# Performance work log

Measured on AMD Instinct MI355X. Metric: run time of the kernel, lower is better.

## Reference

```python
import jax, jax.numpy as jnp
import numpy as np

NEG = float(-2**32 + 1)  # mask fill value used by the original module
H = 8  # number of heads (matches init kwarg h)


def setup_inputs() -> dict:
    key = jax.random.key(0)
    B, S, D, Q, V = 4, 2048, 512, 64, 64
    ks = jax.random.split(key, 10)
    sc = 1.0 / np.sqrt(D)
    x = jax.random.normal(ks[0], (B, S, D), jnp.float32)
    padding_mask = jax.random.randint(ks[1], (B, S), 0, 2, jnp.int32)
    Wq = jax.random.normal(ks[2], (H * Q, D), jnp.float32) * sc
    bq = jnp.zeros((H * Q,), jnp.float32)
    Wk = jax.random.normal(ks[3], (H * Q, D), jnp.float32) * sc
    bk = jnp.zeros((H * Q,), jnp.float32)
    Wv = jax.random.normal(ks[4], (H * V, D), jnp.float32) * sc
    bv = jnp.zeros((H * V,), jnp.float32)
    Wo = jax.random.normal(ks[5], (D, H * V), jnp.float32) * (1.0 / np.sqrt(H * V))
    bo = jnp.zeros((D,), jnp.float32)
    return {"x": x, "padding_mask": padding_mask, "Wq": Wq, "bq": bq,
            "Wk": Wk, "bk": bk, "Wv": Wv, "bv": bv, "Wo": Wo, "bo": bo}


def reference(x, padding_mask, Wq, bq, Wk, bk, Wv, bv, Wo, bo):
    # stage is hardcoded to 'train' (mask=True in init), so the causal branch runs.
    B, S, D = x.shape
    q_dim = Wq.shape[0] // H
    v_dim = Wv.shape[0] // H

    def split_heads(t, d):
        # torch: cat(chunk(h, dim=-1), dim=0) -> head-major [H*B, S, d]
        return t.reshape(B, S, H, d).transpose(2, 0, 1, 3).reshape(H * B, S, d)

    Qh = split_heads(x @ Wq.T + bq, q_dim)   # [H*B, S, q]
    Kh = split_heads(x @ Wk.T + bk, q_dim)
    Vh = split_heads(x @ Wv.T + bv, v_dim)

    score = jnp.einsum('nsd,ntd->nst', Qh, Kh) / jnp.sqrt(jnp.float32(q_dim))  # [H*B,S,S]
    pre_score = score  # module returns the UNMASKED scores (saved before masking)

    # causal mask (mask=True, stage=='train')
    causal = jnp.tril(jnp.ones((S, S), jnp.float32))
    score = jnp.where(causal > 0, score, NEG)

    # padding mask: built batch-major [B*H,S,S] while score is head-major [H*B,...]
    # -- faithful reproduction of the original ordering quirk.
    pm = jnp.broadcast_to(padding_mask[:, None, None, :], (B, H, S, S)).reshape(B * H, S, S)
    score = jnp.where(pm == 0, NEG, score)

    attn = jax.nn.softmax(score, axis=-1)
    out = jnp.einsum('nst,ntd->nsd', attn, Vh)  # [H*B, S, v]

    # torch: cat(chunk(h, dim=0), dim=-1) -> [B, S, H*v]
    heads = out.reshape(H, B, S, v_dim).transpose(1, 2, 0, 3).reshape(B, S, H * v_dim)
    self_attention = heads @ Wo.T + bo
    return self_attention, pre_score
```

## Files before the change

### kernel.cpp

```cpp
#include <hip/hip_runtime.h>
#include <hip/hip_fp16.h>
#include <math.h>

typedef _Float16 f16;
typedef _Float16 f16x8 __attribute__((ext_vector_type(8)));
typedef _Float16 f16x4 __attribute__((ext_vector_type(4)));
typedef float    f32x4 __attribute__((ext_vector_type(4)));

#define MFMA16(a,b,c) __builtin_amdgcn_mfma_f32_16x16x32_f16(a, b, c, 0, 0, 0)

#define MASKNEG (-6.0e9f)
#define DEADTHR (-1.0e9f)
#define LOG2E   1.44269504088896f

__global__ __launch_bounds__(256) void qkv_gemm(
    const float* __restrict__ x,
    const float* __restrict__ Wq, const float* __restrict__ bq,
    const float* __restrict__ Wk, const float* __restrict__ bk,
    const float* __restrict__ Wv, const float* __restrict__ bv,
    f16* __restrict__ Qws, f16* __restrict__ Kws, f16* __restrict__ Vt)
{
    __shared__ f16 Al[128 * 48];
    __shared__ f16 Wl[64 * 48];

    const int tid = threadIdx.x;
    const int bx  = blockIdx.x;
    const int m0  = blockIdx.y * 128;
    const int widx = bx >> 3;
    const int n0   = (bx & 7) * 64;

    const float* W    = (widx == 0) ? Wq : (widx == 1) ? Wk : Wv;
    const float* bias = (widx == 0) ? bq : (widx == 1) ? bk : bv;
    const float scl  = (widx == 0) ? 0.125f : 1.0f;

    const int wid = tid >> 6, lane = tid & 63;
    const int g = lane >> 4, c = lane & 15;
    const int wm = (wid >> 1) * 64, wn = (wid & 1) * 32;
    const int sr = tid >> 3, sc = tid & 7;

    f32x4 acc[4][2] = {};

    for (int kk = 0; kk < 512; kk += 32) {
        __syncthreads();
        #pragma unroll
        for (int rr = 0; rr < 4; ++rr) {
            int row = sr + rr * 32;
            float4 v = *(const float4*)&x[(size_t)(m0 + row) * 512 + kk + sc * 4];
            f16x4 h4 = {(f16)v.x, (f16)v.y, (f16)v.z, (f16)v.w};
            *(f16x4*)&Al[row * 48 + sc * 4] = h4;
        }
        #pragma unroll
        for (int rr = 0; rr < 2; ++rr) {
            int row = sr + rr * 32;
            float4 v = *(const float4*)&W[(size_t)(n0 + row) * 512 + kk + sc * 4];
            f16x4 h4 = {(f16)v.x, (f16)v.y, (f16)v.z, (f16)v.w};
            *(f16x4*)&Wl[row * 48 + sc * 4] = h4;
        }
        __syncthreads();

        f16x8 b0 = *(const f16x8*)&Wl[(wn +  0 + c) * 48 + g * 8];
        f16x8 b1 = *(const f16x8*)&Wl[(wn + 16 + c) * 48 + g * 8];
        #pragma unroll
        for (int mf = 0; mf < 4; ++mf) {
            f16x8 a = *(const f16x8*)&Al[(wm + mf * 16 + c) * 48 + g * 8];
            acc[mf][0] = MFMA16(a, b0, acc[mf][0]);
            acc[mf][1] = MFMA16(a, b1, acc[mf][1]);
        }
    }

    #pragma unroll
    for (int nf = 0; nf < 2; ++nf) {
        int cc = n0 + wn + nf * 16 + c;
        float bval = bias[cc];
        #pragma unroll
        for (int mf = 0; mf < 4; ++mf) {
            if (widx < 2) {
                f16* outp = (widx == 0) ? Qws : Kws;
                #pragma unroll
                for (int r = 0; r < 4; ++r) {
                    int mrow = m0 + wm + mf * 16 + g * 4 + r;
                    outp[(size_t)mrow * 512 + cc] = (f16)((acc[mf][nf][r] + bval) * scl);
                }
            } else {
                int h  = n0 >> 6;
                int d  = wn + nf * 16 + c;
                int t0 = m0 + wm + mf * 16 + g * 4;
                int b  = t0 >> 11;
                int ts = t0 & 2047;
                int nn = h * 4 + b;
                f16x4 pk = {(f16)(acc[mf][nf][0] + bval), (f16)(acc[mf][nf][1] + bval),
                            (f16)(acc[mf][nf][2] + bval), (f16)(acc[mf][nf][3] + bval)};
                *(f16x4*)&Vt[((size_t)(nn * 64 + d)) * 2048 + ts] = pk;
            }
        }
    }
}

__global__ __launch_bounds__(256) void vsum_kernel(
    const f16* __restrict__ Vt, float* __restrict__ Vsum)
{
    const int row  = blockIdx.x * 4 + (threadIdx.x >> 6);
    const int lane = threadIdx.x & 63;
    const f16* p = Vt + (size_t)row * 2048;
    float s = 0.f;
    #pragma unroll
    for (int i = 0; i < 4; ++i) {
        f16x8 v = *(const f16x8*)&p[i * 512 + lane * 8];
        #pragma unroll
        for (int j = 0; j < 8; ++j) s += (float)v[j];
    }
    #pragma unroll
    for (int off = 1; off < 64; off <<= 1) s += __shfl_xor(s, off, 64);
    if (lane == 0) Vsum[row] = s;
}

__global__ __launch_bounds__(256) void attn_kernel(
    const f16* __restrict__ Qws, const f16* __restrict__ Kws,
    const f16* __restrict__ Vt,  const int* __restrict__ pmask,
    const float* __restrict__ Vsum,
    float* __restrict__ pre_score, f16* __restrict__ attn_out)
{
    __shared__ f16 Kl[64 * 72];
    __shared__ f16 Vl[64 * 72];
    __shared__ f16 Pl[4][32 * 72];
    __shared__ float Bias[2048];

    const int tid = threadIdx.x;
    const int wid = tid >> 6, lane = tid & 63;
    const int g = lane >> 4, c = lane & 15;
    const int qt = blockIdx.x;
    const int n  = blockIdx.y;
    const int h = n >> 2, b = n & 3;
    const int pmrow = n >> 3;
    const int qlo = qt * 64 + wid * 16;
    const int qhi = (31 - qt) * 64 + wid * 16;
    const int qrel = wid * 16 + c;

    {
        const int i0 = tid * 8;
        const int4* p4 = (const int4*)(pmask + pmrow * 2048 + i0);
        int4 m0 = p4[0], m1 = p4[1];
        Bias[i0 + 0] = m0.x ? 0.f : MASKNEG;
        Bias[i0 + 1] = m0.y ? 0.f : MASKNEG;
        Bias[i0 + 2] = m0.z ? 0.f : MASKNEG;
        Bias[i0 + 3] = m0.w ? 0.f : MASKNEG;
        Bias[i0 + 4] = m1.x ? 0.f : MASKNEG;
        Bias[i0 + 5] = m1.y ? 0.f : MASKNEG;
        Bias[i0 + 6] = m1.z ? 0.f : MASKNEG;
        Bias[i0 + 7] = m1.w ? 0.f : MASKNEG;
    }

    f16x8 qf[2][2];
    #pragma unroll
    for (int ks = 0; ks < 2; ++ks) {
        qf[0][ks] = *(const f16x8*)
            &Qws[(size_t)(b * 2048 + qlo + c) * 512 + h * 64 + ks * 32 + g * 8];
        qf[1][ks] = *(const f16x8*)
            &Qws[(size_t)(b * 2048 + qhi + c) * 512 + h * 64 + ks * 32 + g * 8];
    }

    f32x4 o[2][4] = {};
    float mrow[2] = {-INFINITY, -INFINITY};
    float lrow[2] = {0.f, 0.f};

    const int sr = tid >> 3, sc = tid & 7;
    const f16* Kbase = Kws + (size_t)(b * 2048) * 512 + h * 64;
    const f16* Vbase = Vt + (size_t)(n * 64) * 2048;
    float* prow0 = pre_score + ((size_t)n * 2048 + qlo + c) * 2048;
    float* prow1 = pre_score + ((size_t)n * 2048 + qhi + c) * 2048;

    const int stageEnd = 32 - qt;

    uint4 ka0, ka1, va0, va1;
    auto glbload = [&](int kt) {
        ka0 = *(const uint4*)&Kbase[(size_t)(kt * 64 + sr) * 512 + sc * 8];
        ka1 = *(const uint4*)&Kbase[(size_t)(kt * 64 + sr + 32) * 512 + sc * 8];
        va0 = *(const uint4*)&Vbase[(size_t)sr * 2048 + kt * 64 + sc * 8];
        va1 = *(const uint4*)&Vbase[(size_t)(sr + 32) * 2048 + kt * 64 + sc * 8];
    };

    glbload(0);
    for (int kt = 0; kt < stageEnd; ++kt) {
        asm volatile("s_waitcnt lgkmcnt(0)" ::: "memory");
        __builtin_amdgcn_s_barrier();
        *(uint4*)&Kl[sr * 72 + sc * 8]        = ka0;
        *(uint4*)&Kl[(sr + 32) * 72 + sc * 8] = ka1;
        *(uint4*)&Vl[sr * 72 + sc * 8]        = va0;
        *(uint4*)&Vl[(sr + 32) * 72 + sc * 8] = va1;
        asm volatile("s_waitcnt lgkmcnt(0)" ::: "memory");
        __builtin_amdgcn_s_barrier();
        if (kt + 1 < stageEnd) glbload(kt + 1);

        f32x4 s2[2][4] = {};
        #pragma unroll
        for (int kc = 0; kc < 4; ++kc)
            #pragma unroll
            for (int ks = 0; ks < 2; ++ks) {
                f16x8 kf = *(const f16x8*)&Kl[(kc * 16 + c) * 72 + ks * 32 + g * 8];
                s2[0][kc] = MFMA16(kf, qf[0][ks], s2[0][kc]);
                s2[1][kc] = MFMA16(kf, qf[1][ks], s2[1][kc]);
            }

        #pragma unroll
        for (int kc = 0; kc < 4; ++kc) {
            *(f32x4*)&prow0[kt * 64 + kc * 16 + g * 4] = s2[0][kc];
            *(f32x4*)&prow1[kt * 64 + kc * 16 + g * 4] = s2[1][kc];
        }

        f32x4 bi[4];
        #pragma unroll
        for (int kc = 0; kc < 4; ++kc)
            bi[kc] = *(const f32x4*)&Bias[kt * 64 + kc * 16 + g * 4];

        const bool L0 = (kt <= qt);
        const bool bnd0 = (kt == qt), bnd1 = (kt == 31 - qt);

        #pragma unroll
        for (int mi = 0; mi < 2; ++mi) {
            if (mi == 0 && !L0) continue;
            const bool bnd = mi ? bnd1 : bnd0;
            float sl[4][4];
            #pragma unroll
            for (int kc = 0; kc < 4; ++kc)
                #pragma unroll
                for (int r = 0; r < 4; ++r) {
                    float sv = s2[mi][kc][r] + bi[kc][r];
                    int klocal = kc * 16 + g * 4 + r;
                    sl[kc][r] = (bnd && klocal > qrel) ? MASKNEG : sv;
                }
            float rm = sl[0][0];
            #pragma unroll
            for (int kc = 0; kc < 4; ++kc)
                #pragma unroll
                for (int r = 0; r < 4; ++r) rm = fmaxf(rm, sl[kc][r]);
            rm = fmaxf(rm, __shfl_xor(rm, 16, 64));
            rm = fmaxf(rm, __shfl_xor(rm, 32, 64));
            float mn = fmaxf(mrow[mi], rm);
            float alpha = exp2f((mrow[mi] - mn) * LOG2E);
            mrow[mi] = mn;
            float ml2 = mn * LOG2E;
            float rs = 0.f;
            #pragma unroll
            for (int kc = 0; kc < 4; ++kc) {
                f16x4 pk;
                #pragma unroll
                for (int r = 0; r < 4; ++r) {
                    float p = exp2f(fmaf(sl[kc][r], LOG2E, -ml2));
                    rs += p;
                    pk[r] = (f16)p;
                }
                *(f16x4*)&Pl[wid][(mi * 16 + c) * 72 + kc * 16 + g * 4] = pk;
            }
            rs += __shfl_xor(rs, 16, 64);
            rs += __shfl_xor(rs, 32, 64);
            lrow[mi] = lrow[mi] * alpha + rs;
            #pragma unroll
            for (int r = 0; r < 4; ++r) {
                float af = __shfl(alpha, g * 4 + r, 64);
                #pragma unroll
                for (int dn = 0; dn < 4; ++dn) o[mi][dn][r] *= af;
            }
        }
        asm volatile("s_waitcnt lgkmcnt(0)" ::: "memory");

        #pragma unroll
        for (int ks = 0; ks < 2; ++ks) {
            f16x8 pa0, pa1;
            if (L0) pa0 = *(const f16x8*)&Pl[wid][( 0 + c) * 72 + ks * 32 + g * 8];
            pa1 = *(const f16x8*)&Pl[wid][(16 + c) * 72 + ks * 32 + g * 8];
            #pragma unroll
            for (int dn = 0; dn < 4; ++dn) {
                f16x8 vb = *(const f16x8*)&Vl[(dn * 16 + c) * 72 + ks * 32 + g * 8];
                if (L0) o[0][dn] = MFMA16(pa0, vb, o[0][dn]);
                o[1][dn] = MFMA16(pa1, vb, o[1][dn]);
            }
        }
    }

    for (int kt = stageEnd; kt < 32; ++kt) {
        f32x4 s2[2][4] = {};
        #pragma unroll
        for (int kc = 0; kc < 4; ++kc)
            #pragma unroll
            for (int ks = 0; ks < 2; ++ks) {
                f16x8 kf = *(const f16x8*)
                    &Kbase[(size_t)(kt * 64 + kc * 16 + c) * 512 + ks * 32 + g * 8];
                s2[0][kc] = MFMA16(kf, qf[0][ks], s2[0][kc]);
                s2[1][kc] = MFMA16(kf, qf[1][ks], s2[1][kc]);
            }
        #pragma unroll
        for (int kc = 0; kc < 4; ++kc) {
            *(f32x4*)&prow0[kt * 64 + kc * 16 + g * 4] = s2[0][kc];
            *(f32x4*)&prow1[kt * 64 + kc * 16 + g * 4] = s2[1][kc];
        }
    }

    #pragma unroll
    for (int mi = 0; mi < 2; ++mi) {
        int qb = mi ? qhi : qlo;
        #pragma unroll
        for (int r = 0; r < 4; ++r) {
            float lo = __shfl(lrow[mi], g * 4 + r, 64);
            float mo = __shfl(mrow[mi], g * 4 + r, 64);
            int srow = qb + g * 4 + r;
            bool dead = (mo < DEADTHR);
            float inv_l = dead ? 0.f : 1.0f / lo;
            #pragma unroll
            for (int dn = 0; dn < 4; ++dn) {
                float val = dead ? Vsum[n * 64 + dn * 16 + c] * (1.0f / 2048.0f)
                                 : o[mi][dn][r] * inv_l;
                attn_out[(size_t)(b * 2048 + srow) * 512 + h * 64 + dn * 16 + c] = (f16)val;
            }
        }
    }
}

__global__ __launch_bounds__(256) void out_gemm(
    const f16* __restrict__ Aattn, const float* __restrict__ Wo,
    const float* __restrict__ bo, float* __restrict__ outp)
{
    __shared__ f16 Al[128 * 48];
    __shared__ f16 Wl[64 * 48];

    const int tid = threadIdx.x;
    const int n0 = blockIdx.x * 64;
    const int m0 = blockIdx.y * 128;
    const int wid = tid >> 6, lane = tid & 63;
    const int g = lane >> 4, c = lane & 15;
    const int wm = (wid >> 1) * 64, wn = (wid & 1) * 32;

    const int sr4 = tid >> 2, sc4 = tid & 3;
    const int sr8 = tid >> 3, sc8 = tid & 7;

    f32x4 acc[4][2] = {};

    for (int kk = 0; kk < 512; kk += 32) {
        __syncthreads();
        #pragma unroll
        for (int rr = 0; rr < 2; ++rr) {
            int row = sr4 + rr * 64;
            *(uint4*)&Al[row * 48 + sc4 * 8] =
                *(const uint4*)&Aattn[(size_t)(m0 + row) * 512 + kk + sc4 * 8];
        }
        #pragma unroll
        for (int rr = 0; rr < 2; ++rr) {
            int row = sr8 + rr * 32;
            float4 v = *(const float4*)&Wo[(size_t)(n0 + row) * 512 + kk + sc8 * 4];
            f16x4 h4 = {(f16)v.x, (f16)v.y, (f16)v.z, (f16)v.w};
            *(f16x4*)&Wl[row * 48 + sc8 * 4] = h4;
        }
        __syncthreads();

        f16x8 b0 = *(const f16x8*)&Wl[(wn +  0 + c) * 48 + g * 8];
        f16x8 b1 = *(const f16x8*)&Wl[(wn + 16 + c) * 48 + g * 8];
        #pragma unroll
        for (int mf = 0; mf < 4; ++mf) {
            f16x8 a = *(const f16x8*)&Al[(wm + mf * 16 + c) * 48 + g * 8];
            acc[mf][0] = MFMA16(a, b0, acc[mf][0]);
            acc[mf][1] = MFMA16(a, b1, acc[mf][1]);
        }
    }

    #pragma unroll
    for (int nf = 0; nf < 2; ++nf) {
        int cc = n0 + wn + nf * 16 + c;
        float bval = bo[cc];
        #pragma unroll
        for (int mf = 0; mf < 4; ++mf)
            #pragma unroll
            for (int r = 0; r < 4; ++r)
                outp[(size_t)(m0 + wm + mf * 16 + g * 4 + r) * 512 + cc] =
                    acc[mf][nf][r] + bval;
    }
}

extern "C" void kernel_launch(void* const* d_in, const int* in_sizes, int n_in,
                              void* d_out, int out_size, void* d_ws, size_t ws_size,
                              hipStream_t stream)
{
    (void)in_sizes; (void)n_in; (void)out_size; (void)ws_size;

    const float* x  = (const float*)d_in[0];
    const int*   pm = (const int*)  d_in[1];
    const float* Wq = (const float*)d_in[2];
    const float* bq = (const float*)d_in[3];
    const float* Wk = (const float*)d_in[4];
    const float* bk = (const float*)d_in[5];
    const float* Wv = (const float*)d_in[6];
    const float* bv = (const float*)d_in[7];
    const float* Wo = (const float*)d_in[8];
    const float* bo = (const float*)d_in[9];

    float* out = (float*)d_out;
    float* pre = out + (size_t)4 * 2048 * 512;

    f16*   Qws  = (f16*)d_ws;
    f16*   Kws  = Qws + (size_t)8192 * 512;
    f16*   Vt   = Kws + (size_t)8192 * 512;
    f16*   Aat  = Vt  + (size_t)2048 * 2048;
    float* Vsum = (float*)(Aat + (size_t)8192 * 512);

    qkv_gemm   <<<dim3(24, 64), 256, 0, stream>>>(x, Wq, bq, Wk, bk, Wv, bv, Qws, Kws, Vt);
    vsum_kernel<<<dim3(512),    256, 0, stream>>>(Vt, Vsum);
    attn_kernel<<<dim3(16, 32), 256, 0, stream>>>(Qws, Kws, Vt, pm, Vsum, pre, Aat);
    out_gemm   <<<dim3(8, 64),  256, 0, stream>>>(Aat, Wo, bo, out);
}
```

Measured before the change: 286.0 us.

## Split attention KV loop across two blocks and merge partials in combine kernel

The attention kernel gains a z-dimension of 2, so each block handles every other key tile (split-K / flash-decoding style), doubling the grid from 512 to 1024 blocks. Each block writes unnormalized fp16 partial outputs plus per-row max and sum into a workspace, and a new combine kernel rescales and merges them, applying the dead-row Vsum fallback. Softmax+PV is refactored into a per-row-chunk lambda with a smaller P buffer, and launch bounds request 3 blocks per SM. This aims to fill the GPU better at the cost of an extra kernel launch, partial-buffer traffic, fp16 rounding of unnormalized partials, and per-block setup (bias, Q load) being repeated.

```diff
diff --git a/kernel.cpp b/kernel.cpp
--- a/kernel.cpp
+++ b/kernel.cpp
@@ -114,15 +114,14 @@
     if (lane == 0) Vsum[row] = s;
 }
 
-__global__ __launch_bounds__(256) void attn_kernel(
+__global__ __launch_bounds__(256, 3) void attn_kernel(
     const f16* __restrict__ Qws, const f16* __restrict__ Kws,
     const f16* __restrict__ Vt,  const int* __restrict__ pmask,
-    const float* __restrict__ Vsum,
-    float* __restrict__ pre_score, f16* __restrict__ attn_out)
+    float* __restrict__ pre_score, f16* __restrict__ part)
 {
     __shared__ f16 Kl[64 * 72];
     __shared__ f16 Vl[64 * 72];
-    __shared__ f16 Pl[4][32 * 72];
+    __shared__ f16 Pl[4][16 * 72];
     __shared__ float Bias[2048];
 
     const int tid = threadIdx.x;
@@ -130,6 +129,7 @@
     const int g = lane >> 4, c = lane & 15;
     const int qt = blockIdx.x;
     const int n  = blockIdx.y;
+    const int p  = blockIdx.z;
     const int h = n >> 2, b = n & 3;
     const int pmrow = n >> 3;
     const int qlo = qt * 64 + wid * 16;
@@ -179,8 +179,63 @@
         va1 = *(const uint4*)&Vbase[(size_t)(sr + 32) * 2048 + kt * 64 + sc * 8];
     };
 
-    glbload(0);
-    for (int kt = 0; kt < stageEnd; ++kt) {
+    auto chunk_sm_pv = [&](int mi, bool bnd, const f32x4* s2c, const f32x4* bi)
+        __attribute__((always_inline)) {
+        float sl[4][4];
+        #pragma unroll
+        for (int kc = 0; kc < 4; ++kc)
+            #pragma unroll
+            for (int r = 0; r < 4; ++r) {
+                float sv = s2c[kc][r] + bi[kc][r];
+                int klocal = kc * 16 + g * 4 + r;
+                sl[kc][r] = (bnd && klocal > qrel) ? MASKNEG : sv;
+            }
+        float rm = sl[0][0];
+        #pragma unroll
+        for (int kc = 0; kc < 4; ++kc)
+            #pragma unroll
+            for (int r = 0; r < 4; ++r) rm = fmaxf(rm, sl[kc][r]);
+        rm = fmaxf(rm, __shfl_xor(rm, 16, 64));
+        rm = fmaxf(rm, __shfl_xor(rm, 32, 64));
+        float mn = fmaxf(mrow[mi], rm);
+        float alpha = exp2f((mrow[mi] - mn) * LOG2E);
+        mrow[mi] = mn;
+        float ml2 = mn * LOG2E;
+        float rs = 0.f;
+        #pragma unroll
+        for (int kc = 0; kc < 4; ++kc) {
+            f16x4 pk;
+            #pragma unroll
+            for (int r = 0; r < 4; ++r) {
+                float pe = exp2f(fmaf(sl[kc][r], LOG2E, -ml2));
+                rs += pe;
+                pk[r] = (f16)pe;
+            }
+            *(f16x4*)&Pl[wid][c * 72 + kc * 16 + g * 4] = pk;
+        }
+        rs += __shfl_xor(rs, 16, 64);
+        rs += __shfl_xor(rs, 32, 64);
+        lrow[mi] = lrow[mi] * alpha + rs;
+        #pragma unroll
+        for (int r = 0; r < 4; ++r) {
+            float af = __shfl(alpha, g * 4 + r, 64);
+            #pragma unroll
+            for (int dn = 0; dn < 4; ++dn) o[mi][dn][r] *= af;
+        }
+        asm volatile("s_waitcnt lgkmcnt(0)" ::: "memory");
+        #pragma unroll
+        for (int ks = 0; ks < 2; ++ks) {
+            f16x8 pa = *(const f16x8*)&Pl[wid][c * 72 + ks * 32 + g * 8];
+            #pragma unroll
+            for (int dn = 0; dn < 4; ++dn) {
+                f16x8 vb = *(const f16x8*)&Vl[(dn * 16 + c) * 72 + ks * 32 + g * 8];
+                o[mi][dn] = MFMA16(pa, vb, o[mi][dn]);
+            }
+        }
+    };
+
+    glbload(p);
+    for (int kt = p; kt < stageEnd; kt += 2) {
         asm volatile("s_waitcnt lgkmcnt(0)" ::: "memory");
         __builtin_amdgcn_s_barrier();
         *(uint4*)&Kl[sr * 72 + sc * 8]        = ka0;
@@ -189,7 +244,7 @@
         *(uint4*)&Vl[(sr + 32) * 72 + sc * 8] = va1;
         asm volatile("s_waitcnt lgkmcnt(0)" ::: "memory");
         __builtin_amdgcn_s_barrier();
-        if (kt + 1 < stageEnd) glbload(kt + 1);
+        if (kt + 2 < stageEnd) glbload(kt + 2);
 
         f32x4 s2[2][4] = {};
         #pragma unroll
@@ -213,71 +268,12 @@
             bi[kc] = *(const f32x4*)&Bias[kt * 64 + kc * 16 + g * 4];
 
         const bool L0 = (kt <= qt);
-        const bool bnd0 = (kt == qt), bnd1 = (kt == 31 - qt);
-
-        #pragma unroll
-        for (int mi = 0; mi < 2; ++mi) {
-            if (mi == 0 && !L0) continue;
-            const bool bnd = mi ? bnd1 : bnd0;
-            float sl[4][4];
-            #pragma unroll
-            for (int kc = 0; kc < 4; ++kc)
-                #pragma unroll
-                for (int r = 0; r < 4; ++r) {
-                    float sv = s2[mi][kc][r] + bi[kc][r];
-                    int klocal = kc * 16 + g * 4 + r;
-                    sl[kc][r] = (bnd && klocal > qrel) ? MASKNEG : sv;
-                }
-            float rm = sl[0][0];
-            #pragma unroll
-            for (int kc = 0; kc < 4; ++kc)
-                #pragma unroll
-                for (int r = 0; r < 4; ++r) rm = fmaxf(rm, sl[kc][r]);
-            rm = fmaxf(rm, __shfl_xor(rm, 16, 64));
-            rm = fmaxf(rm, __shfl_xor(rm, 32, 64));
-            float mn = fmaxf(mrow[mi], rm);
-            float alpha = exp2f((mrow[mi] - mn) * LOG2E);
-            mrow[mi] = mn;
-            float ml2 = mn * LOG2E;
-            float rs = 0.f;
-            #pragma unroll
-            for (int kc = 0; kc < 4; ++kc) {
-                f16x4 pk;
-                #pragma unroll
-                for (int r = 0; r < 4; ++r) {
-                    float p = exp2f(fmaf(sl[kc][r], LOG2E, -ml2));
-                    rs += p;
-                    pk[r] = (f16)p;
-                }
-                *(f16x4*)&Pl[wid][(mi * 16 + c) * 72 + kc * 16 + g * 4] = pk;
-            }
-            rs += __shfl_xor(rs, 16, 64);
-            rs += __shfl_xor(rs, 32, 64);
-            lrow[mi] = lrow[mi] * alpha + rs;
-            #pragma unroll
-            for (int r = 0; r < 4; ++r) {
-                float af = __shfl(alpha, g * 4 + r, 64);
-                #pragma unroll
-                for (int dn = 0; dn < 4; ++dn) o[mi][dn][r] *= af;
-            }
-        }
+        if (L0) chunk_sm_pv(0, kt == qt, s2[0], bi);
         asm volatile("s_waitcnt lgkmcnt(0)" ::: "memory");
-
-        #pragma unroll
-        for (int ks = 0; ks < 2; ++ks) {
-            f16x8 pa0, pa1;
-            if (L0) pa0 = *(const f16x8*)&Pl[wid][( 0 + c) * 72 + ks * 32 + g * 8];
-            pa1 = *(const f16x8*)&Pl[wid][(16 + c) * 72 + ks * 32 + g * 8];
-            #pragma unroll
-            for (int dn = 0; dn < 4; ++dn) {
-                f16x8 vb = *(const f16x8*)&Vl[(dn * 16 + c) * 72 + ks * 32 + g * 8];
-                if (L0) o[0][dn] = MFMA16(pa0, vb, o[0][dn]);
-                o[1][dn] = MFMA16(pa1, vb, o[1][dn]);
-            }
-        }
-    }
-
-    for (int kt = stageEnd; kt < 32; ++kt) {
+        chunk_sm_pv(1, kt == 31 - qt, s2[1], bi);
+    }
+
+    for (int kt = stageEnd + ((stageEnd ^ p) & 1); kt < 32; kt += 2) {
         f32x4 s2[2][4] = {};
         #pragma unroll
         for (int kc = 0; kc < 4; ++kc)
@@ -295,24 +291,64 @@
         }
     }
 
+    f16* pb = part + (size_t)p * 65536 * 72;
     #pragma unroll
     for (int mi = 0; mi < 2; ++mi) {
-        int qb = mi ? qhi : qlo;
-        #pragma unroll
-        for (int r = 0; r < 4; ++r) {
-            float lo = __shfl(lrow[mi], g * 4 + r, 64);
-            float mo = __shfl(mrow[mi], g * 4 + r, 64);
-            int srow = qb + g * 4 + r;
-            bool dead = (mo < DEADTHR);
-            float inv_l = dead ? 0.f : 1.0f / lo;
-            #pragma unroll
-            for (int dn = 0; dn < 4; ++dn) {
-                float val = dead ? Vsum[n * 64 + dn * 16 + c] * (1.0f / 2048.0f)
-                                 : o[mi][dn][r] * inv_l;
-                attn_out[(size_t)(b * 2048 + srow) * 512 + h * 64 + dn * 16 + c] = (f16)val;
-            }
-        }
-    }
+        size_t rowbase = (size_t)n * 2048 + (mi ? qhi : qlo);
+        #pragma unroll
+        for (int r = 0; r < 4; ++r)
+            #pragma unroll
+            for (int dn = 0; dn < 4; ++dn)
+                pb[(rowbase + g * 4 + r) * 72 + dn * 16 + c] = (f16)o[mi][dn][r];
+        if (g == 0) {
+            float* pf = (float*)&pb[(rowbase + c) * 72 + 64];
+            pf[0] = mrow[mi];
+            pf[1] = lrow[mi];
+        }
+    }
+}
+
+__global__ __launch_bounds__(256) void combine_kernel(
+    const f16* __restrict__ part, const float* __restrict__ Vsum,
+    f16* __restrict__ Aat)
+{
+    const int t  = threadIdx.x;
+    const int R  = blockIdx.x * 64 + (t >> 2);
+    const int dg = (t & 3) * 16;
+    const int n = R >> 11, q = R & 2047;
+    const int h = n >> 2, b = n & 3;
+    const f16* p0 = part + (size_t)R * 72;
+    const f16* p1 = part + ((size_t)65536 + R) * 72;
+    const float* ml0 = (const float*)(p0 + 64);
+    const float* ml1 = (const float*)(p1 + 64);
+    float m0 = ml0[0], l0 = ml0[1];
+    float m1 = ml1[0], l1 = ml1[1];
+    float m = fmaxf(m0, m1);
+    f16* outp = Aat + ((size_t)(b * 2048 + q)) * 512 + h * 64 + dg;
+    f16x8 r0, r1;
+    if (m < DEADTHR) {
+        const float* vs = Vsum + n * 64 + dg;
+        #pragma unroll
+        for (int i = 0; i < 8; ++i) {
+            r0[i] = (f16)(vs[i] * (1.0f / 2048.0f));
+            r1[i] = (f16)(vs[8 + i] * (1.0f / 2048.0f));
+        }
+    } else {
+        float w0 = (m0 < DEADTHR) ? 0.f : exp2f((m0 - m) * LOG2E);
+        float w1 = (m1 < DEADTHR) ? 0.f : exp2f((m1 - m) * LOG2E);
+        float invl = 1.0f / (l0 * w0 + l1 * w1);
+        f16x8 a0 = *(const f16x8*)&p0[dg];
+        f16x8 a1 = *(const f16x8*)&p0[dg + 8];
+        f16x8 c0 = *(const f16x8*)&p1[dg];
+        f16x8 c1 = *(const f16x8*)&p1[dg + 8];
+        #pragma unroll
+        for (int i = 0; i < 8; ++i) {
+            r0[i] = (f16)(((float)a0[i] * w0 + (float)c0[i] * w1) * invl);
+            r1[i] = (f16)(((float)a1[i] * w0 + (float)c1[i] * w1) * invl);
+        }
+    }
+    *(f16x8*)outp = r0;
+    *(f16x8*)(outp + 8) = r1;
 }
 
 __global__ __launch_bounds__(256) void out_gemm(
@@ -399,9 +435,11 @@
     f16*   Vt   = Kws + (size_t)8192 * 512;
     f16*   Aat  = Vt  + (size_t)2048 * 2048;
     float* Vsum = (float*)(Aat + (size_t)8192 * 512);
+    f16*   part = (f16*)(Vsum + 2048);
 
     qkv_gemm   <<<dim3(24, 64), 256, 0, stream>>>(x, Wq, bq, Wk, bk, Wv, bv, Qws, Kws, Vt);
     vsum_kernel<<<dim3(512),    256, 0, stream>>>(Vt, Vsum);
-    attn_kernel<<<dim3(16, 32), 256, 0, stream>>>(Qws, Kws, Vt, pm, Vsum, pre, Aat);
+    attn_kernel<<<dim3(16, 32, 2), 256, 0, stream>>>(Qws, Kws, Vt, pm, pre, part);
+    combine_kernel<<<dim3(1024), 256, 0, stream>>>(part, Vsum, Aat);
     out_gemm   <<<dim3(8, 64),  256, 0, stream>>>(Aat, Wo, bo, out);
 }
```

Result: slower. 300.7 us (+5.1%).

## Split pre_score writing into separate blocks interleaved with attention blocks

Applied to the files above, without the earlier changes.

Attention blocks no longer write the unmasked score matrix. Instead, 8 of every 9 blocks in a single fused grid recompute QK^T tiles and stream them to pre_score, while every 9th block runs flash attention. The aim is to separate the store-bound pre_score traffic from the MFMA/softmax work and spread it across many more blocks. The cost is that QK^T is computed twice.

```diff
diff --git a/kernel.cpp b/kernel.cpp
--- a/kernel.cpp
+++ b/kernel.cpp
@@ -114,7 +114,7 @@
     if (lane == 0) Vsum[row] = s;
 }
 
-__global__ __launch_bounds__(256) void attn_kernel(
+__global__ __launch_bounds__(256) void fat_kernel(
     const f16* __restrict__ Qws, const f16* __restrict__ Kws,
     const f16* __restrict__ Vt,  const int* __restrict__ pmask,
     const float* __restrict__ Vsum,
@@ -125,11 +125,49 @@
     __shared__ f16 Pl[4][32 * 72];
     __shared__ float Bias[2048];
 
+    const int bid = blockIdx.x;
     const int tid = threadIdx.x;
     const int wid = tid >> 6, lane = tid & 63;
     const int g = lane >> 4, c = lane & 15;
-    const int qt = blockIdx.x;
-    const int n  = blockIdx.y;
+
+    if (bid % 9 != 0) {
+        const int sid = bid - bid / 9 - 1;
+        const int n  = sid >> 7;
+        const int q0 = ((sid >> 3) & 15) * 128;
+        const int t0 = (sid & 7) * 256 + wid * 64;
+        const int h = n >> 2, b = n & 3;
+
+        const f16* Qbase = Qws + (size_t)(b * 2048) * 512 + h * 64;
+        const f16* Kbase = Kws + (size_t)(b * 2048) * 512 + h * 64;
+        float* prow = pre_score + ((size_t)n * 2048 + q0 + c) * 2048;
+
+        f16x8 qf[8][2];
+        #pragma unroll
+        for (int qi = 0; qi < 8; ++qi)
+            #pragma unroll
+            for (int ks = 0; ks < 2; ++ks)
+                qf[qi][ks] = *(const f16x8*)
+                    &Qbase[(size_t)(q0 + qi * 16 + c) * 512 + ks * 32 + g * 8];
+
+        #pragma unroll
+        for (int tf = 0; tf < 4; ++tf) {
+            const int t = t0 + tf * 16;
+            f16x8 kf0 = *(const f16x8*)&Kbase[(size_t)(t + c) * 512 + g * 8];
+            f16x8 kf1 = *(const f16x8*)&Kbase[(size_t)(t + c) * 512 + 32 + g * 8];
+            #pragma unroll
+            for (int qi = 0; qi < 8; ++qi) {
+                f32x4 acc = {};
+                acc = MFMA16(kf0, qf[qi][0], acc);
+                acc = MFMA16(kf1, qf[qi][1], acc);
+                *(f32x4*)&prow[(size_t)(qi * 16) * 2048 + t + g * 4] = acc;
+            }
+        }
+        return;
+    }
+
+    const int fid = bid / 9;
+    const int qt = fid & 15;
+    const int n  = fid >> 4;
     const int h = n >> 2, b = n & 3;
     const int pmrow = n >> 3;
     const int qlo = qt * 64 + wid * 16;
@@ -166,8 +204,6 @@
     const int sr = tid >> 3, sc = tid & 7;
     const f16* Kbase = Kws + (size_t)(b * 2048) * 512 + h * 64;
     const f16* Vbase = Vt + (size_t)(n * 64) * 2048;
-    float* prow0 = pre_score + ((size_t)n * 2048 + qlo + c) * 2048;
-    float* prow1 = pre_score + ((size_t)n * 2048 + qhi + c) * 2048;
 
     const int stageEnd = 32 - qt;
 
@@ -201,12 +237,6 @@
                 s2[1][kc] = MFMA16(kf, qf[1][ks], s2[1][kc]);
             }
 
-        #pragma unroll
-        for (int kc = 0; kc < 4; ++kc) {
-            *(f32x4*)&prow0[kt * 64 + kc * 16 + g * 4] = s2[0][kc];
-            *(f32x4*)&prow1[kt * 64 + kc * 16 + g * 4] = s2[1][kc];
-        }
-
         f32x4 bi[4];
         #pragma unroll
         for (int kc = 0; kc < 4; ++kc)
@@ -277,24 +307,6 @@
         }
     }
 
-    for (int kt = stageEnd; kt < 32; ++kt) {
-        f32x4 s2[2][4] = {};
-        #pragma unroll
-        for (int kc = 0; kc < 4; ++kc)
-            #pragma unroll
-            for (int ks = 0; ks < 2; ++ks) {
-                f16x8 kf = *(const f16x8*)
-                    &Kbase[(size_t)(kt * 64 + kc * 16 + c) * 512 + ks * 32 + g * 8];
-                s2[0][kc] = MFMA16(kf, qf[0][ks], s2[0][kc]);
-                s2[1][kc] = MFMA16(kf, qf[1][ks], s2[1][kc]);
-            }
-        #pragma unroll
-        for (int kc = 0; kc < 4; ++kc) {
-            *(f32x4*)&prow0[kt * 64 + kc * 16 + g * 4] = s2[0][kc];
-            *(f32x4*)&prow1[kt * 64 + kc * 16 + g * 4] = s2[1][kc];
-        }
-    }
-
     #pragma unroll
     for (int mi = 0; mi < 2; ++mi) {
         int qb = mi ? qhi : qlo;
@@ -402,6 +414,6 @@
 
     qkv_gemm   <<<dim3(24, 64), 256, 0, stream>>>(x, Wq, bq, Wk, bk, Wv, bv, Qws, Kws, Vt);
     vsum_kernel<<<dim3(512),    256, 0, stream>>>(Vt, Vsum);
-    attn_kernel<<<dim3(16, 32), 256, 0, stream>>>(Qws, Kws, Vt, pm, Vsum, pre, Aat);
+    fat_kernel <<<dim3(4608),   256, 0, stream>>>(Qws, Kws, Vt, pm, Vsum, pre, Aat);
     out_gemm   <<<dim3(8, 64),  256, 0, stream>>>(Aat, Wo, bo, out);
 }
```

Result: slower. 380.3 us (+33.0%).

## Split pre-score output into a dedicated streaming score kernel separate from flash attention

Applied to the files above, without the earlier changes.

The unmasked score matrix write is moved out of the fused attention kernel into a separate kernel that recomputes QK^T across all key tiles and streams the results with nontemporal stores. The flash kernel now only does the masked softmax and PV product, so it no longer carries the heavy global score stores or the non-causal tail loop. In exchange, QK^T for the causal half is computed twice, and Q/K are read again by a separate launch.

```diff
diff --git a/kernel.cpp b/kernel.cpp
--- a/kernel.cpp
+++ b/kernel.cpp
@@ -114,11 +114,10 @@
     if (lane == 0) Vsum[row] = s;
 }
 
-__global__ __launch_bounds__(256) void attn_kernel(
+__global__ __launch_bounds__(256) void flash_kernel(
     const f16* __restrict__ Qws, const f16* __restrict__ Kws,
     const f16* __restrict__ Vt,  const int* __restrict__ pmask,
-    const float* __restrict__ Vsum,
-    float* __restrict__ pre_score, f16* __restrict__ attn_out)
+    const float* __restrict__ Vsum, f16* __restrict__ attn_out)
 {
     __shared__ f16 Kl[64 * 72];
     __shared__ f16 Vl[64 * 72];
@@ -166,8 +165,6 @@
     const int sr = tid >> 3, sc = tid & 7;
     const f16* Kbase = Kws + (size_t)(b * 2048) * 512 + h * 64;
     const f16* Vbase = Vt + (size_t)(n * 64) * 2048;
-    float* prow0 = pre_score + ((size_t)n * 2048 + qlo + c) * 2048;
-    float* prow1 = pre_score + ((size_t)n * 2048 + qhi + c) * 2048;
 
     const int stageEnd = 32 - qt;
 
@@ -201,12 +198,6 @@
                 s2[1][kc] = MFMA16(kf, qf[1][ks], s2[1][kc]);
             }
 
-        #pragma unroll
-        for (int kc = 0; kc < 4; ++kc) {
-            *(f32x4*)&prow0[kt * 64 + kc * 16 + g * 4] = s2[0][kc];
-            *(f32x4*)&prow1[kt * 64 + kc * 16 + g * 4] = s2[1][kc];
-        }
-
         f32x4 bi[4];
         #pragma unroll
         for (int kc = 0; kc < 4; ++kc)
@@ -277,24 +268,6 @@
         }
     }
 
-    for (int kt = stageEnd; kt < 32; ++kt) {
-        f32x4 s2[2][4] = {};
-        #pragma unroll
-        for (int kc = 0; kc < 4; ++kc)
-            #pragma unroll
-            for (int ks = 0; ks < 2; ++ks) {
-                f16x8 kf = *(const f16x8*)
-                    &Kbase[(size_t)(kt * 64 + kc * 16 + c) * 512 + ks * 32 + g * 8];
-                s2[0][kc] = MFMA16(kf, qf[0][ks], s2[0][kc]);
-                s2[1][kc] = MFMA16(kf, qf[1][ks], s2[1][kc]);
-            }
-        #pragma unroll
-        for (int kc = 0; kc < 4; ++kc) {
-            *(f32x4*)&prow0[kt * 64 + kc * 16 + g * 4] = s2[0][kc];
-            *(f32x4*)&prow1[kt * 64 + kc * 16 + g * 4] = s2[1][kc];
-        }
-    }
-
     #pragma unroll
     for (int mi = 0; mi < 2; ++mi) {
         int qb = mi ? qhi : qlo;
@@ -312,6 +285,46 @@
                 attn_out[(size_t)(b * 2048 + srow) * 512 + h * 64 + dn * 16 + c] = (f16)val;
             }
         }
+    }
+}
+
+__global__ __launch_bounds__(256) void score_kernel(
+    const f16* __restrict__ Qws, const f16* __restrict__ Kws,
+    float* __restrict__ pre_score)
+{
+    const int tid = threadIdx.x;
+    const int wid = tid >> 6, lane = tid & 63;
+    const int g = lane >> 4, c = lane & 15;
+    const int n  = blockIdx.y;
+    const int h = n >> 2, b = n & 3;
+    const int qb0 = blockIdx.x * 128 + wid * 32;
+    const int qb1 = qb0 + 16;
+
+    const f16* Qbase = Qws + (size_t)(b * 2048) * 512 + h * 64;
+    const f16* Kbase = Kws + (size_t)(b * 2048) * 512 + h * 64;
+
+    f16x8 qf0[2], qf1[2];
+    #pragma unroll
+    for (int ks = 0; ks < 2; ++ks) {
+        qf0[ks] = *(const f16x8*)&Qbase[(size_t)(qb0 + c) * 512 + ks * 32 + g * 8];
+        qf1[ks] = *(const f16x8*)&Qbase[(size_t)(qb1 + c) * 512 + ks * 32 + g * 8];
+    }
+
+    float* prow0 = pre_score + ((size_t)n * 2048 + qb0 + c) * 2048;
+    float* prow1 = pre_score + ((size_t)n * 2048 + qb1 + c) * 2048;
+
+    #pragma unroll 4
+    for (int t0 = 0; t0 < 2048; t0 += 16) {
+        const f16* kp = &Kbase[(size_t)(t0 + c) * 512 + g * 8];
+        f16x8 kf0 = *(const f16x8*)kp;
+        f16x8 kf1 = *(const f16x8*)(kp + 32);
+        f32x4 s0 = {}, s1 = {};
+        s0 = MFMA16(kf0, qf0[0], s0);
+        s0 = MFMA16(kf1, qf0[1], s0);
+        s1 = MFMA16(kf0, qf1[0], s1);
+        s1 = MFMA16(kf1, qf1[1], s1);
+        __builtin_nontemporal_store(s0, (f32x4*)&prow0[t0 + g * 4]);
+        __builtin_nontemporal_store(s1, (f32x4*)&prow1[t0 + g * 4]);
     }
 }
 
@@ -400,8 +413,9 @@
     f16*   Aat  = Vt  + (size_t)2048 * 2048;
     float* Vsum = (float*)(Aat + (size_t)8192 * 512);
 
-    qkv_gemm   <<<dim3(24, 64), 256, 0, stream>>>(x, Wq, bq, Wk, bk, Wv, bv, Qws, Kws, Vt);
-    vsum_kernel<<<dim3(512),    256, 0, stream>>>(Vt, Vsum);
-    attn_kernel<<<dim3(16, 32), 256, 0, stream>>>(Qws, Kws, Vt, pm, Vsum, pre, Aat);
-    out_gemm   <<<dim3(8, 64),  256, 0, stream>>>(Aat, Wo, bo, out);
-}
+    qkv_gemm    <<<dim3(24, 64), 256, 0, stream>>>(x, Wq, bq, Wk, bk, Wv, bv, Qws, Kws, Vt);
+    vsum_kernel <<<dim3(512),    256, 0, stream>>>(Vt, Vsum);
+    flash_kernel<<<dim3(16, 32), 256, 0, stream>>>(Qws, Kws, Vt, pm, Vsum, Aat);
+    score_kernel<<<dim3(16, 32), 256, 0, stream>>>(Qws, Kws, pre);
+    out_gemm    <<<dim3(8, 64),  256, 0, stream>>>(Aat, Wo, bo, out);
+}
```

Measured after the change: 373.2 us. +30.5%, slower.
